# Performance work log

Hardware: AMD Instinct MI355X
Metric: run time of the kernel (lower is better)

The kernel has to match this reference:

```python
import jax, jax.numpy as jnp
import numpy as np

HID = 256
HEADS = 8
HD = HID // HEADS  # head_dim = 32


def setup_inputs() -> dict:
    key = jax.random.key(0)
    ks = jax.random.split(key, 16)
    B, N = 4, 2048
    s = 0.02
    inp = {
        'x': jax.random.normal(ks[0], (B, N, 4, HID), dtype=jnp.float32),
        'Wq': jax.random.normal(ks[1], (HID, HID), dtype=jnp.float32) * s,
        'bq': jnp.zeros((HID,), jnp.float32),
        'Wk': jax.random.normal(ks[2], (HID, HID), dtype=jnp.float32) * s,
        'bk': jnp.zeros((HID,), jnp.float32),
        'Wv': jax.random.normal(ks[3], (HID, HID), dtype=jnp.float32) * s,
        'bv': jnp.zeros((HID,), jnp.float32),
        'Wvec': jax.random.normal(ks[4], (2 * HID, HID), dtype=jnp.float32) * s,
        'Wo': jax.random.normal(ks[5], (3 * HID, HID), dtype=jnp.float32) * s,
        'bo': jnp.zeros((3 * HID,), jnp.float32),
        'Wg': jax.random.normal(ks[6], (HID, 2 * HID), dtype=jnp.float32) * s,
        'bg': jnp.zeros((HID,), jnp.float32),
        'alpha_dot': jnp.asarray(1.0, jnp.float32),
        'alpha_norm': jnp.asarray(1.0, jnp.float32),
    }
    return inp


def reference(x, Wq, bq, Wk, bk, Wv, bv, Wvec, Wo, bo, Wg, bg, alpha_dot, alpha_norm):
    B, N, _, H = x.shape
    nh, hd = HEADS, HD
    x_scalar = x[:, :, 0]          # (B,N,H)
    vec = x[:, :, 1:]              # (B,N,3,H)

    def lin(a, W, b=None):
        y = a @ W.T
        return y + b if b is not None else y

    # scalar q/k/v -> (B,heads,N,hd)
    q = lin(x_scalar, Wq, bq).reshape(B, N, nh, hd).transpose(0, 2, 1, 3)
    k = lin(x_scalar, Wk, bk).reshape(B, N, nh, hd).transpose(0, 2, 1, 3)
    v = lin(x_scalar, Wv, bv).reshape(B, N, nh, hd).transpose(0, 2, 1, 3)

    # invariant features from vector channels
    vec_proj = lin(vec, Wvec)                  # (B,N,3,2H)
    vec1, vec2 = vec_proj[..., :H], vec_proj[..., H:]
    vec_dot = jnp.sum(vec1 * vec2, axis=-2)    # (B,N,H)
    vec_norm = jnp.linalg.norm(vec, axis=2)    # (B,N,H)

    # equivariant values: (B,heads,N,3*hd)
    vec_v = vec.reshape(B, N, 3, nh, hd).transpose(0, 3, 1, 2, 4).reshape(B, nh, N, 3 * hd)

    # fused attention: one softmax, aggregate scalar v and vector v together
    scale = 1.0 / np.sqrt(hd).astype(np.float32)
    scores = jnp.einsum('bhqd,bhkd->bhqk', q, k) * scale
    attn = jax.nn.softmax(scores, axis=-1)
    v_all = jnp.concatenate([v, vec_v], axis=-1)        # (B,h,N,4*hd)
    out_all = jnp.einsum('bhqk,bhkd->bhqd', attn, v_all)
    out_s, out_v = out_all[..., :hd], out_all[..., hd:]

    x_out = out_s.transpose(0, 2, 1, 3).reshape(B, N, H)
    vec_aggr = out_v.reshape(B, nh, N, 3, hd).transpose(0, 2, 3, 1, 4).reshape(B, N, 3, H)

    invariants = jnp.concatenate([alpha_dot * vec_dot, alpha_norm * vec_norm], axis=-1)
    gate = jax.nn.sigmoid(lin(invariants, Wg, bg))[:, :, None, :]  # (B,N,1,H)
    vec_combined = gate * vec_aggr + vec  # vector_mixing='add', gating=True

    o = lin(x_out, Wo, bo)
    o1, o2, o3 = o[..., :H], o[..., H:2 * H], o[..., 2 * H:]
    x_updated = vec_dot * o1 + vec_norm * o2 + o3

    x_final = jnp.concatenate([x_updated[:, :, None, :], vec_combined], axis=2)  # (B,N,4,H)
    return x_final
```

## Files before the change

kernel.cpp:

```cpp
#include <hip/hip_runtime.h>
#include <cstdint>
#include <cstddef>

#define HIDN 256
#define NHEAD 8
#define HD 32
#define NSEQ 2048
#define QS (0.17677669529663687f * 1.4426950408889634f)

typedef __attribute__((ext_vector_type(8))) short short8;
typedef __attribute__((ext_vector_type(4))) short short4v;
typedef __attribute__((ext_vector_type(4))) float f32x4;

static __device__ __forceinline__ short f2bf(float f) {
    union { float f; uint32_t u; } v; v.f = f;
    uint32_t r = (v.u + 0x7FFF + ((v.u >> 16) & 1)) >> 16;
    return (short)r;
}
static __device__ __forceinline__ float bf2f(short s) {
    union { uint32_t u; float f; } v; v.u = ((uint32_t)(uint16_t)s) << 16;
    return v.f;
}

static __device__ __forceinline__ float ex2(float x) {
#if defined(__has_builtin)
#if __has_builtin(__builtin_amdgcn_exp2f)
    return __builtin_amdgcn_exp2f(x);
#else
    return exp2f(x);
#endif
#else
    return exp2f(x);
#endif
}

static __device__ __forceinline__ uint32_t pkbf16(float lo, float hi) {
    uint32_t r;
    asm("v_cvt_pk_bf16_f32 %0, %1, %2" : "=v"(r) : "v"(lo), "v"(hi));
    return r;
}

static __device__ __forceinline__ void gload16(const void* g, void* l) {
    __builtin_amdgcn_global_load_lds(
        (__attribute__((address_space(1))) void*)g,
        (__attribute__((address_space(3))) void*)l, 16, 0, 0);
}

__global__ __launch_bounds__(256) void wcvt_kernel(
    const float* __restrict__ Wq, const float* __restrict__ Wk,
    const float* __restrict__ Wv, const float* __restrict__ Wvec,
    const float* __restrict__ Wo, const float* __restrict__ Wg,
    const float* __restrict__ bq, const float* __restrict__ bk,
    const float* __restrict__ bv,
    const float* __restrict__ ad, const float* __restrict__ an,
    short* __restrict__ Wqkvb, short* __restrict__ Wvecb,
    short* __restrict__ Wob, short* __restrict__ Wgb, float* __restrict__ bqkvs)
{
    int idx = blockIdx.x * 256 + threadIdx.x;
    if (idx < 65536)        Wqkvb[idx] = f2bf(Wq[idx] * QS);
    else if (idx < 131072)  Wqkvb[idx] = f2bf(Wk[idx - 65536]);
    else if (idx < 196608)  Wqkvb[idx] = f2bf(Wv[idx - 131072]);
    else if (idx < 327680)  Wvecb[idx - 196608] = f2bf(Wvec[idx - 196608]);
    else if (idx < 524288)  Wob[idx - 327680] = f2bf(Wo[idx - 327680]);
    else {
        int i2 = idx - 524288;
        int k = i2 & 511;
        float s = (k < 256) ? ad[0] : an[0];
        Wgb[i2] = f2bf(Wg[i2] * s);
    }
    if (idx < 256)          bqkvs[idx] = bq[idx] * QS;
    else if (idx < 512)     bqkvs[idx] = bk[idx - 256];
    else if (idx < 768)     bqkvs[idx] = bv[idx - 512];
}

__global__ __launch_bounds__(256) void qkv_kernel(
    const float* __restrict__ x, const short* __restrict__ Wqkvb,
    const float* __restrict__ bqkvs,
    short* __restrict__ qbf, short* __restrict__ kbf, short* __restrict__ vtb)
{
    __shared__ short xs[32 * 264];
    __shared__ short vtmp[256 * 34];
    const int tid = threadIdx.x;
    const int m0 = blockIdx.x * 32;
    const int b  = m0 >> 11;
    const int n0 = m0 & 2047;

    #pragma unroll
    for (int l = 0; l < 8; l++) {
        int i = l * 256 + tid;
        int t = i >> 6, j4 = i & 63;
        float4 v = *(const float4*)(x + (size_t)(m0 + t) * 1024 + j4 * 4);
        short4v s = { f2bf(v.x), f2bf(v.y), f2bf(v.z), f2bf(v.w) };
        *(short4v*)&xs[t * 264 + j4 * 4] = s;
    }
    __syncthreads();

    const int wave = tid >> 6, lane = tid & 63;
    const int col = lane & 15, quad = lane >> 4;

    short8 xf[2][8];
    #pragma unroll
    for (int mt = 0; mt < 2; mt++)
        #pragma unroll
        for (int kk = 0; kk < 8; kk++)
            xf[mt][kk] = *(const short8*)&xs[(mt * 16 + col) * 264 + kk * 32 + quad * 8];

    #pragma unroll
    for (int y = 0; y < 3; y++) {
        f32x4 acc[2][4];
        #pragma unroll
        for (int mt = 0; mt < 2; mt++)
            #pragma unroll
            for (int nt = 0; nt < 4; nt++) acc[mt][nt] = (f32x4){0.f,0.f,0.f,0.f};

        const short* Wb = Wqkvb + (size_t)(y * 256 + wave * 64) * 256;
        #pragma unroll
        for (int kk = 0; kk < 8; kk++) {
            #pragma unroll
            for (int nt = 0; nt < 4; nt++) {
                short8 wf = *(const short8*)(Wb + (size_t)(nt * 16 + col) * 256 + kk * 32 + quad * 8);
                #pragma unroll
                for (int mt = 0; mt < 2; mt++)
                    acc[mt][nt] = __builtin_amdgcn_mfma_f32_16x16x32_bf16(wf, xf[mt][kk], acc[mt][nt], 0, 0, 0);
            }
        }

        if (y < 2) {
            short* dst = (y == 0) ? qbf : kbf;
            #pragma unroll
            for (int nt = 0; nt < 4; nt++) {
                int ch = wave * 64 + nt * 16 + quad * 4;
                float4 bi = *(const float4*)&bqkvs[y * 256 + ch];
                int h = ch >> 5, d = ch & 31;
                #pragma unroll
                for (int mt = 0; mt < 2; mt++) {
                    int n = n0 + mt * 16 + col;
                    short4v s = { f2bf(acc[mt][nt][0] + bi.x), f2bf(acc[mt][nt][1] + bi.y),
                                  f2bf(acc[mt][nt][2] + bi.z), f2bf(acc[mt][nt][3] + bi.w) };
                    int dd = (y == 1) ? (((d >> 3) ^ ((n >> 1) & 3)) * 8 + (d & 7)) : d;
                    *(short4v*)(dst + ((size_t)(b * 8 + h) * 2048 + n) * 32 + dd) = s;
                }
            }
        } else {
            #pragma unroll
            for (int nt = 0; nt < 4; nt++) {
                int ch = wave * 64 + nt * 16 + quad * 4;
                float4 bi = *(const float4*)&bqkvs[512 + ch];
                #pragma unroll
                for (int mt = 0; mt < 2; mt++) {
                    int tok = mt * 16 + col;
                    vtmp[(ch + 0) * 34 + tok] = f2bf(acc[mt][nt][0] + bi.x);
                    vtmp[(ch + 1) * 34 + tok] = f2bf(acc[mt][nt][1] + bi.y);
                    vtmp[(ch + 2) * 34 + tok] = f2bf(acc[mt][nt][2] + bi.z);
                    vtmp[(ch + 3) * 34 + tok] = f2bf(acc[mt][nt][3] + bi.w);
                }
            }
        }
    }
    __syncthreads();
    {
        int ch = tid;
        short s[32];
        #pragma unroll
        for (int t = 0; t < 32; t++) s[t] = vtmp[ch * 34 + t];
        int h = ch >> 5, d = ch & 31;
        size_t tile = (size_t)(b * 8 + h) * 32 + (n0 >> 6);
        short* dst = vtb + (tile * 128 + d) * 64;
        int gb = (n0 >> 3) & 4;
        #pragma unroll
        for (int g = 0; g < 4; g++)
            *(short8*)(dst + (((gb + g) ^ (d & 7)) * 8)) = *(short8*)&s[g * 8];
    }
}

__global__ __launch_bounds__(512) void vec_kernel(
    const float* __restrict__ x, const short* __restrict__ Wvecb,
    float* __restrict__ dotb, short* __restrict__ invb,
    float* __restrict__ normb, short* __restrict__ vtb)
{
    __shared__ short vb[3 * 16 * 264];
    const int tid = threadIdx.x;
    const int m0 = blockIdx.x * 16;
    const int b = m0 >> 11, n0 = m0 & 2047;

    #pragma unroll
    for (int p = 0; p < 6; p++) {
        int f4 = p * 512 + tid;
        int t = f4 / 192;
        int rem = f4 - t * 192;
        int c = rem >> 6, j4 = rem & 63;
        float4 v = *(const float4*)(x + (size_t)(m0 + t) * 1024 + 256 + c * 256 + j4 * 4);
        short4v s = { f2bf(v.x), f2bf(v.y), f2bf(v.z), f2bf(v.w) };
        *(short4v*)&vb[(c * 16 + t) * 264 + j4 * 4] = s;
    }
    __syncthreads();

    const int wave = tid >> 6, lane = tid & 63;
    const int col = lane & 15, quad = lane >> 4;
    const int j0 = wave * 32;

    f32x4 d1[3][2], d2[3][2];
    #pragma unroll
    for (int c = 0; c < 3; c++)
        #pragma unroll
        for (int nt = 0; nt < 2; nt++) {
            d1[c][nt] = (f32x4){0.f,0.f,0.f,0.f};
            d2[c][nt] = (f32x4){0.f,0.f,0.f,0.f};
        }

    #pragma unroll
    for (int kk = 0; kk < 8; kk++) {
        short8 w1[2], w2[2];
        #pragma unroll
        for (int nt = 0; nt < 2; nt++) {
            w1[nt] = *(const short8*)&Wvecb[(size_t)(j0 + nt * 16 + col) * 256 + kk * 32 + quad * 8];
            w2[nt] = *(const short8*)&Wvecb[(size_t)(256 + j0 + nt * 16 + col) * 256 + kk * 32 + quad * 8];
        }
        #pragma unroll
        for (int c = 0; c < 3; c++) {
            short8 xf = *(const short8*)&vb[(c * 16 + col) * 264 + kk * 32 + quad * 8];
            #pragma unroll
            for (int nt = 0; nt < 2; nt++) {
                d1[c][nt] = __builtin_amdgcn_mfma_f32_16x16x32_bf16(w1[nt], xf, d1[c][nt], 0, 0, 0);
                d2[c][nt] = __builtin_amdgcn_mfma_f32_16x16x32_bf16(w2[nt], xf, d2[c][nt], 0, 0, 0);
            }
        }
    }
    #pragma unroll
    for (int nt = 0; nt < 2; nt++) {
        f32x4 dac = d1[0][nt] * d2[0][nt] + d1[1][nt] * d2[1][nt] + d1[2][nt] * d2[2][nt];
        float4 o = { dac[0], dac[1], dac[2], dac[3] };
        *(float4*)&dotb[(size_t)(m0 + col) * 256 + j0 + nt * 16 + quad * 4] = o;
        short4v s = { f2bf(dac[0]), f2bf(dac[1]), f2bf(dac[2]), f2bf(dac[3]) };
        *(short4v*)&invb[(size_t)(m0 + col) * 512 + j0 + nt * 16 + quad * 4] = s;
    }

    const int j = tid & 255, tp = tid >> 8;
    const int h = j >> 5, d = j & 31;
    #pragma unroll
    for (int t8 = 0; t8 < 8; t8++) {
        int t = tp * 8 + t8;
        float v0 = bf2f(vb[(0 * 16 + t) * 264 + j]);
        float v1 = bf2f(vb[(1 * 16 + t) * 264 + j]);
        float v2 = bf2f(vb[(2 * 16 + t) * 264 + j]);
        float nm = sqrtf(v0 * v0 + v1 * v1 + v2 * v2);
        normb[(size_t)(m0 + t) * 256 + j] = nm;
        invb[(size_t)(m0 + t) * 512 + 256 + j] = f2bf(nm);
    }
    {
        size_t tile = (size_t)(b * 8 + h) * 32 + (n0 >> 6);
        int gg = ((n0 & 63) >> 3) + tp;
        #pragma unroll
        for (int c = 0; c < 3; c++) {
            short8 s;
            #pragma unroll
            for (int t8 = 0; t8 < 8; t8++) s[t8] = vb[(c * 16 + tp * 8 + t8) * 264 + j];
            int row = 32 + c * 32 + d;
            *(short8*)(vtb + (tile * 128 + row) * 64 + ((gg ^ (d & 7)) * 8)) = s;
        }
    }
}

__global__ __launch_bounds__(256) void attn_kernel(
    const short* __restrict__ qb, const short* __restrict__ kb,
    const short* __restrict__ vtb,
    short* __restrict__ xob, short* __restrict__ ovb)
{
    __shared__ short Ks[2][64 * 32];
    __shared__ short Vs[2][128 * 64];
    __shared__ short Pl[4][2][16 * 40];
    const int tid = threadIdx.x;
    const int wave = tid >> 6, lane = tid & 63;
    const int col = lane & 15, quad = lane >> 4;

    const int D = blockIdx.x;
    const int slot = D >> 3;
    const int bh = (D & 7) + ((slot & 3) << 3);
    const int qt = slot >> 2;
    const int m0 = qt * 128 + wave * 32;
    const int b = bh >> 3, h = bh & 7;

    const short* qbase = qb + (size_t)bh * NSEQ * HD;
    const short* ksrc  = kb + (size_t)bh * NSEQ * HD;
    const short* vsrc  = vtb + (size_t)bh * 32 * 8192;

    short8 qfrag[2];
    #pragma unroll
    for (int s = 0; s < 2; s++)
        qfrag[s] = *(const short8*)(qbase + (size_t)(m0 + s * 16 + col) * 32 + quad * 8);

    f32x4 o[2][8];
    #pragma unroll
    for (int s = 0; s < 2; s++)
        #pragma unroll
        for (int dt = 0; dt < 8; dt++) o[s][dt] = (f32x4){0.f,0.f,0.f,0.f};
    float lrun[2] = {0.f, 0.f};

    const int wb = (tid & 192) * 8;

    auto STAGE = [&](int buf, int t) {
        const short* kp = ksrc + (size_t)t * 2048 + tid * 8;
        gload16(kp, &Ks[buf][wb]);
        const short* vp = vsrc + (size_t)t * 8192 + tid * 8;
        #pragma unroll
        for (int p = 0; p < 4; p++)
            gload16(vp + p * 2048, &Vs[buf][p * 2048 + wb]);
    };

    const int ksw  = (quad ^ ((col >> 1) & 3)) * 8;
    const int vsw0 = (quad ^ (col & 7)) * 8;
    const int vsw1 = ((quad + 4) ^ (col & 7)) * 8;

    STAGE(0, 0);
    __syncthreads();

    for (int kt = 0; kt < 32; kt++) {
        const int cur = kt & 1;
        if (kt < 31) STAGE(cur ^ 1, kt + 1);

        short8 kf[4];
        #pragma unroll
        for (int nt = 0; nt < 4; nt++)
            kf[nt] = *(const short8*)&Ks[cur][(nt * 16 + col) * 32 + ksw];

        #pragma unroll
        for (int s = 0; s < 2; s++) {
            f32x4 sc[4];
            #pragma unroll
            for (int nt = 0; nt < 4; nt++)
                sc[nt] = __builtin_amdgcn_mfma_f32_16x16x32_bf16(
                    kf[nt], qfrag[s], (f32x4){0.f,0.f,0.f,0.f}, 0, 0, 0);
            float rs = 0.f;
            short* pd = &Pl[wave][s][col * 40];
            #pragma unroll
            for (int nt = 0; nt < 4; nt++) {
                float p0 = ex2(sc[nt][0]), p1 = ex2(sc[nt][1]);
                float p2 = ex2(sc[nt][2]), p3 = ex2(sc[nt][3]);
                rs += (p0 + p1) + (p2 + p3);
                uint2 w = { pkbf16(p0, p1), pkbf16(p2, p3) };
                *(uint2*)(pd + nt * 16 + quad * 4) = w;
            }
            lrun[s] += rs;
        }

        #pragma unroll
        for (int c = 0; c < 2; c++) {
            short8 pa[2];
            #pragma unroll
            for (int s = 0; s < 2; s++)
                pa[s] = *(const short8*)&Pl[wave][s][col * 40 + c * 32 + quad * 8];
            const int vsw = c ? vsw1 : vsw0;
            #pragma unroll
            for (int dt = 0; dt < 8; dt++) {
                short8 vf = *(const short8*)&Vs[cur][(dt * 16 + col) * 64 + vsw];
                #pragma unroll
                for (int s = 0; s < 2; s++)
                    o[s][dt] = __builtin_amdgcn_mfma_f32_16x16x32_bf16(vf, pa[s], o[s][dt], 0, 0, 0);
            }
        }
        __syncthreads();
    }

    #pragma unroll
    for (int s = 0; s < 2; s++) {
        float l = lrun[s];
        l += __shfl_xor(l, 16);
        l += __shfl_xor(l, 32);
        float linv = 1.0f / l;

        size_t mg = (size_t)b * 2048 + m0 + s * 16 + col;
        short* xr = xob + mg * 256 + h * 32;
        #pragma unroll
        for (int dt = 0; dt < 2; dt++) {
            short4v sv = { f2bf(o[s][dt][0] * linv), f2bf(o[s][dt][1] * linv),
                           f2bf(o[s][dt][2] * linv), f2bf(o[s][dt][3] * linv) };
            *(short4v*)(xr + dt * 16 + quad * 4) = sv;
        }
        short* vr = ovb + mg * 768 + h * 32;
        #pragma unroll
        for (int dt = 2; dt < 8; dt++) {
            int c = (dt - 2) >> 1, d2 = ((dt - 2) & 1) * 16 + quad * 4;
            short4v sv = { f2bf(o[s][dt][0] * linv), f2bf(o[s][dt][1] * linv),
                           f2bf(o[s][dt][2] * linv), f2bf(o[s][dt][3] * linv) };
            *(short4v*)(vr + c * 256 + d2) = sv;
        }
    }
}

__global__ __launch_bounds__(256, 2) void ogemm_kernel(
    const float* __restrict__ x, const short* __restrict__ xob,
    const short* __restrict__ invb,
    const float* __restrict__ dotb, const float* __restrict__ normb,
    const short* __restrict__ ovb,
    const short* __restrict__ Wob, const short* __restrict__ Wgb,
    const float* __restrict__ bo, const float* __restrict__ bg,
    float* __restrict__ out)
{
    __shared__ __align__(16) union {
        struct { short inv[16 * 520]; short xo[16 * 264]; } in;
        struct { short gate[16 * 264]; short o[16 * 776]; } ob;
    } u;
    const int tid = threadIdx.x;
    const int M0 = blockIdx.x * 16;

    #pragma unroll
    for (int l = 0; l < 4; l++) {
        int i = l * 256 + tid;
        int m = i >> 6, seg = i & 63;
        *(short8*)&u.in.inv[m * 520 + seg * 8] =
            *(const short8*)(invb + (size_t)(M0 + m) * 512 + seg * 8);
    }
    #pragma unroll
    for (int l = 0; l < 2; l++) {
        int i = l * 256 + tid;
        int m = i >> 5, seg = i & 31;
        *(short8*)&u.in.xo[m * 264 + seg * 8] =
            *(const short8*)(xob + (size_t)(M0 + m) * 256 + seg * 8);
    }
    __syncthreads();

    const int wave = tid >> 6, lane = tid & 63;
    const int col = lane & 15, quad = lane >> 4;

    f32x4 acc[16];
    #pragma unroll
    for (int nt = 0; nt < 16; nt++) acc[nt] = (f32x4){0.f,0.f,0.f,0.f};

    if (wave == 0) {
        short8 wbuf[2][16];
        #pragma unroll
        for (int nt = 0; nt < 16; nt++)
            wbuf[0][nt] = *(const short8*)(Wgb + (size_t)(nt * 16 + col) * 512 + quad * 8);
        #pragma unroll
        for (int kk = 0; kk < 16; kk++) {
            if (kk < 15) {
                #pragma unroll
                for (int nt = 0; nt < 16; nt++)
                    wbuf[(kk + 1) & 1][nt] =
                        *(const short8*)(Wgb + (size_t)(nt * 16 + col) * 512 + (kk + 1) * 32 + quad * 8);
            }
            short8 xf = *(const short8*)&u.in.inv[col * 520 + kk * 32 + quad * 8];
            #pragma unroll
            for (int nt = 0; nt < 16; nt++)
                acc[nt] = __builtin_amdgcn_mfma_f32_16x16x32_bf16(wbuf[kk & 1][nt], xf, acc[nt], 0, 0, 0);
        }
    } else {
        const short* Wb = Wob + (size_t)(wave - 1) * 256 * 256;
        short8 wbuf[2][16];
        #pragma unroll
        for (int nt = 0; nt < 16; nt++)
            wbuf[0][nt] = *(const short8*)(Wb + (size_t)(nt * 16 + col) * 256 + quad * 8);
        #pragma unroll
        for (int kk = 0; kk < 8; kk++) {
            if (kk < 7) {
                #pragma unroll
                for (int nt = 0; nt < 16; nt++)
                    wbuf[(kk + 1) & 1][nt] =
                        *(const short8*)(Wb + (size_t)(nt * 16 + col) * 256 + (kk + 1) * 32 + quad * 8);
            }
            short8 xf = *(const short8*)&u.in.xo[col * 264 + kk * 32 + quad * 8];
            #pragma unroll
            for (int nt = 0; nt < 16; nt++)
                acc[nt] = __builtin_amdgcn_mfma_f32_16x16x32_bf16(wbuf[kk & 1][nt], xf, acc[nt], 0, 0, 0);
        }
    }
    __syncthreads();

    if (wave == 0) {
        #pragma unroll
        for (int nt = 0; nt < 16; nt++) {
            int ch = nt * 16 + quad * 4;
            float4 bi = *(const float4*)&bg[ch];
            short4v s = { f2bf(1.f / (1.f + __expf(-(acc[nt][0] + bi.x)))),
                          f2bf(1.f / (1.f + __expf(-(acc[nt][1] + bi.y)))),
                          f2bf(1.f / (1.f + __expf(-(acc[nt][2] + bi.z)))),
                          f2bf(1.f / (1.f + __expf(-(acc[nt][3] + bi.w)))) };
            *(short4v*)&u.ob.gate[col * 264 + ch] = s;
        }
    } else {
        #pragma unroll
        for (int nt = 0; nt < 16; nt++) {
            int ch = (wave - 1) * 256 + nt * 16 + quad * 4;
            float4 bi = *(const float4*)&bo[ch];
            short4v s = { f2bf(acc[nt][0] + bi.x), f2bf(acc[nt][1] + bi.y),
                          f2bf(acc[nt][2] + bi.z), f2bf(acc[nt][3] + bi.w) };
            *(short4v*)&u.ob.o[col * 776 + ch] = s;
        }
    }
    __syncthreads();

    #pragma unroll
    for (int l = 0; l < 16; l++) {
        int idx4 = l * 256 + tid;
        int m = idx4 >> 8;
        int j = (idx4 & 255) * 4;
        size_t mg = (size_t)(M0 + m);
        if (j < 256) {
            float4 dv = *(const float4*)(dotb + mg * 256 + j);
            float4 nv = *(const float4*)(normb + mg * 256 + j);
            short4v o1 = *(short4v*)&u.ob.o[m * 776 + j];
            short4v o2 = *(short4v*)&u.ob.o[m * 776 + 256 + j];
            short4v o3 = *(short4v*)&u.ob.o[m * 776 + 512 + j];
            float4 r;
            r.x = dv.x * bf2f(o1[0]) + nv.x * bf2f(o2[0]) + bf2f(o3[0]);
            r.y = dv.y * bf2f(o1[1]) + nv.y * bf2f(o2[1]) + bf2f(o3[1]);
            r.z = dv.z * bf2f(o1[2]) + nv.z * bf2f(o2[2]) + bf2f(o3[2]);
            r.w = dv.w * bf2f(o1[3]) + nv.w * bf2f(o2[3]) + bf2f(o3[3]);
            *(float4*)(out + mg * 1024 + j) = r;
        } else {
            int c = (j >> 8) - 1, jj = j & 255;
            short4v g4 = *(short4v*)&u.ob.gate[m * 264 + jj];
            short4v av4 = *(const short4v*)(ovb + mg * 768 + c * 256 + jj);
            float4 xv = *(const float4*)(x + mg * 1024 + 256 + c * 256 + jj);
            float4 r = { bf2f(g4[0]) * bf2f(av4[0]) + xv.x, bf2f(g4[1]) * bf2f(av4[1]) + xv.y,
                         bf2f(g4[2]) * bf2f(av4[2]) + xv.z, bf2f(g4[3]) * bf2f(av4[3]) + xv.w };
            *(float4*)(out + mg * 1024 + j) = r;
        }
    }
}

extern "C" void kernel_launch(void* const* d_in, const int* in_sizes, int n_in,
                              void* d_out, int out_size, void* d_ws, size_t ws_size,
                              hipStream_t stream)
{
    const float* x    = (const float*)d_in[0];
    const float* Wq   = (const float*)d_in[1];
    const float* bq   = (const float*)d_in[2];
    const float* Wk   = (const float*)d_in[3];
    const float* bk   = (const float*)d_in[4];
    const float* Wv   = (const float*)d_in[5];
    const float* bv   = (const float*)d_in[6];
    const float* Wvec = (const float*)d_in[7];
    const float* Wo   = (const float*)d_in[8];
    const float* bo   = (const float*)d_in[9];
    const float* Wg   = (const float*)d_in[10];
    const float* bg   = (const float*)d_in[11];
    const float* adp  = (const float*)d_in[12];
    const float* anp  = (const float*)d_in[13];
    float* out = (float*)d_out;

    float* ws    = (float*)d_ws;
    short* qbf   = (short*)ws;
    short* kbf   = (short*)(ws + 1048576);
    short* vtb   = (short*)(ws + 2097152);
    float* dotb  = ws + 6291456;
    float* normb = ws + 8388608;
    short* xob   = (short*)(ws + 10485760);
    short* ovb   = (short*)(ws + 11534336);
    short* invb  = (short*)(ws + 17825792);
    short* Wqkvb = (short*)(ws + 19922944);
    float* bqkvs = ws + 20021248;
    short* Wvecb = (short*)(ws + 20022016);
    short* Wob   = (short*)(ws + 20087552);
    short* Wgb   = (short*)(ws + 20185856);

    wcvt_kernel<<<2560, 256, 0, stream>>>(Wq, Wk, Wv, Wvec, Wo, Wg, bq, bk, bv,
                                          adp, anp, Wqkvb, Wvecb, Wob, Wgb, bqkvs);
    qkv_kernel<<<256, 256, 0, stream>>>(x, Wqkvb, bqkvs, qbf, kbf, vtb);
    vec_kernel<<<512, 512, 0, stream>>>(x, Wvecb, dotb, invb, normb, vtb);
    attn_kernel<<<512, 256, 0, stream>>>(qbf, kbf, vtb, xob, ovb);
    ogemm_kernel<<<512, 256, 0, stream>>>(x, xob, invb, dotb, normb, ovb,
                                          Wob, Wgb, bo, bg, out);
}
```

Measured before the change: 269.0 us.

## Switch attention to 32x32x16 MFMA with register-resident P via permlane swap

Attention now uses 32x32x16 bf16 MFMA instead of 16x16x32. K and V are pre-laid-out in fragment order by the producer kernels, so each lane loads its operand directly from LDS with no swizzle. The softmax probabilities are repacked in registers using v_permlane32_swap instead of a round trip through LDS, which removes the Pl buffer and its LDS traffic. The trade-off is higher accumulator register pressure and strict dependence on the new K/V layout matching the MFMA operand mapping.

Result: faster. 259.7 us (-3.4%).

```diff
diff --git a/kernel.cpp b/kernel.cpp
--- a/kernel.cpp
+++ b/kernel.cpp
@@ -11,6 +11,8 @@
 typedef __attribute__((ext_vector_type(8))) short short8;
 typedef __attribute__((ext_vector_type(4))) short short4v;
 typedef __attribute__((ext_vector_type(4))) float f32x4;
+typedef __attribute__((ext_vector_type(16))) float f32x16;
+typedef __attribute__((ext_vector_type(4))) uint32_t u32x4;
 
 static __device__ __forceinline__ short f2bf(float f) {
     union { float f; uint32_t u; } v; v.f = f;
@@ -40,10 +42,23 @@
     return r;
 }
 
+static __device__ __forceinline__ void half_bcast(uint32_t x, uint32_t& lo, uint32_t& hi) {
+    uint32_t a = x, b = x;
+    asm("v_permlane32_swap_b32 %0, %1" : "+v"(a), "+v"(b));
+    lo = a; hi = b;
+}
+
 static __device__ __forceinline__ void gload16(const void* g, void* l) {
     __builtin_amdgcn_global_load_lds(
         (__attribute__((address_space(1))) void*)g,
         (__attribute__((address_space(3))) void*)l, 16, 0, 0);
+}
+
+static __device__ __forceinline__ f32x16 zero16() {
+    f32x16 z;
+    #pragma unroll
+    for (int i = 0; i < 16; i++) z[i] = 0.f;
+    return z;
 }
 
 __global__ __launch_bounds__(256) void wcvt_kernel(
@@ -125,20 +140,36 @@
             }
         }
 
-        if (y < 2) {
-            short* dst = (y == 0) ? qbf : kbf;
+        if (y == 0) {
             #pragma unroll
             for (int nt = 0; nt < 4; nt++) {
                 int ch = wave * 64 + nt * 16 + quad * 4;
-                float4 bi = *(const float4*)&bqkvs[y * 256 + ch];
+                float4 bi = *(const float4*)&bqkvs[ch];
                 int h = ch >> 5, d = ch & 31;
                 #pragma unroll
                 for (int mt = 0; mt < 2; mt++) {
                     int n = n0 + mt * 16 + col;
                     short4v s = { f2bf(acc[mt][nt][0] + bi.x), f2bf(acc[mt][nt][1] + bi.y),
                                   f2bf(acc[mt][nt][2] + bi.z), f2bf(acc[mt][nt][3] + bi.w) };
-                    int dd = (y == 1) ? (((d >> 3) ^ ((n >> 1) & 3)) * 8 + (d & 7)) : d;
-                    *(short4v*)(dst + ((size_t)(b * 8 + h) * 2048 + n) * 32 + dd) = s;
+                    *(short4v*)(qbf + ((size_t)(b * 8 + h) * 2048 + n) * 32 + d) = s;
+                }
+            }
+        } else if (y == 1) {
+            #pragma unroll
+            for (int nt = 0; nt < 4; nt++) {
+                int ch = wave * 64 + nt * 16 + quad * 4;
+                float4 bi = *(const float4*)&bqkvs[256 + ch];
+                int h = ch >> 5, d = ch & 31;
+                #pragma unroll
+                for (int mt = 0; mt < 2; mt++) {
+                    int n = n0 + mt * 16 + col;
+                    short4v s = { f2bf(acc[mt][nt][0] + bi.x), f2bf(acc[mt][nt][1] + bi.y),
+                                  f2bf(acc[mt][nt][2] + bi.z), f2bf(acc[mt][nt][3] + bi.w) };
+                    int f  = ((n & 63) >> 5) * 2 + (d >> 4);
+                    int lk = (n & 31) + (((d >> 3) & 1) << 5);
+                    short* dst = kbf + ((size_t)(b * 8 + h) * 32 + (n >> 6)) * 2048
+                               + f * 512 + lk * 8 + (d & 7);
+                    *(short4v*)dst = s;
                 }
             }
         } else {
@@ -165,11 +196,14 @@
         for (int t = 0; t < 32; t++) s[t] = vtmp[ch * 34 + t];
         int h = ch >> 5, d = ch & 31;
         size_t tile = (size_t)(b * 8 + h) * 32 + (n0 >> 6);
-        short* dst = vtb + (tile * 128 + d) * 64;
-        int gb = (n0 >> 3) & 4;
-        #pragma unroll
-        for (int g = 0; g < 4; g++)
-            *(short8*)(dst + (((gb + g) ^ (d & 7)) * 8)) = *(short8*)&s[g * 8];
+        short* dst = vtb + tile * 8192;
+        #pragma unroll
+        for (int g = 0; g < 4; g++) {
+            int kbse = (n0 & 63) + g * 8;
+            int f = kbse >> 4;
+            int h2 = (kbse >> 3) & 1;
+            *(short8*)(dst + f * 512 + (d + h2 * 32) * 8) = *(short8*)&s[g * 8];
+        }
     }
 }
 
@@ -249,14 +283,15 @@
     }
     {
         size_t tile = (size_t)(b * 8 + h) * 32 + (n0 >> 6);
-        int gg = ((n0 & 63) >> 3) + tp;
+        int kbse = (n0 & 63) + tp * 8;
+        int ks = kbse >> 4, h2 = (kbse >> 3) & 1;
         #pragma unroll
         for (int c = 0; c < 3; c++) {
             short8 s;
             #pragma unroll
             for (int t8 = 0; t8 < 8; t8++) s[t8] = vb[(c * 16 + tp * 8 + t8) * 264 + j];
-            int row = 32 + c * 32 + d;
-            *(short8*)(vtb + (tile * 128 + row) * 64 + ((gg ^ (d & 7)) * 8)) = s;
+            int f = (1 + c) * 4 + ks;
+            *(short8*)(vtb + tile * 8192 + f * 512 + (d + h2 * 32) * 8) = s;
         }
     }
 }
@@ -266,12 +301,11 @@
     const short* __restrict__ vtb,
     short* __restrict__ xob, short* __restrict__ ovb)
 {
-    __shared__ short Ks[2][64 * 32];
-    __shared__ short Vs[2][128 * 64];
-    __shared__ short Pl[4][2][16 * 40];
+    __shared__ short Ks[2][2048];
+    __shared__ short Vs[2][8192];
     const int tid = threadIdx.x;
     const int wave = tid >> 6, lane = tid & 63;
-    const int col = lane & 15, quad = lane >> 4;
+    const int q32 = lane & 31, hi = lane >> 5;
 
     const int D = blockIdx.x;
     const int slot = D >> 3;
@@ -281,35 +315,26 @@
     const int b = bh >> 3, h = bh & 7;
 
     const short* qbase = qb + (size_t)bh * NSEQ * HD;
-    const short* ksrc  = kb + (size_t)bh * NSEQ * HD;
+    const short* ksrc  = kb + (size_t)bh * 32 * 2048;
     const short* vsrc  = vtb + (size_t)bh * 32 * 8192;
 
     short8 qfrag[2];
     #pragma unroll
-    for (int s = 0; s < 2; s++)
-        qfrag[s] = *(const short8*)(qbase + (size_t)(m0 + s * 16 + col) * 32 + quad * 8);
-
-    f32x4 o[2][8];
-    #pragma unroll
-    for (int s = 0; s < 2; s++)
-        #pragma unroll
-        for (int dt = 0; dt < 8; dt++) o[s][dt] = (f32x4){0.f,0.f,0.f,0.f};
-    float lrun[2] = {0.f, 0.f};
-
-    const int wb = (tid & 192) * 8;
+    for (int ks = 0; ks < 2; ks++)
+        qfrag[ks] = *(const short8*)(qbase + (size_t)(m0 + q32) * 32 + ks * 16 + hi * 8);
+
+    f32x16 o[4];
+    #pragma unroll
+    for (int dt = 0; dt < 4; dt++) o[dt] = zero16();
+    float lrun = 0.f;
 
     auto STAGE = [&](int buf, int t) {
-        const short* kp = ksrc + (size_t)t * 2048 + tid * 8;
-        gload16(kp, &Ks[buf][wb]);
+        gload16(ksrc + (size_t)t * 2048 + tid * 8, &Ks[buf][wave * 512]);
         const short* vp = vsrc + (size_t)t * 8192 + tid * 8;
         #pragma unroll
         for (int p = 0; p < 4; p++)
-            gload16(vp + p * 2048, &Vs[buf][p * 2048 + wb]);
+            gload16(vp + p * 2048, &Vs[buf][p * 2048 + wave * 512]);
     };
-
-    const int ksw  = (quad ^ ((col >> 1) & 3)) * 8;
-    const int vsw0 = (quad ^ (col & 7)) * 8;
-    const int vsw1 = ((quad + 4) ^ (col & 7)) * 8;
 
     STAGE(0, 0);
     __syncthreads();
@@ -318,71 +343,70 @@
         const int cur = kt & 1;
         if (kt < 31) STAGE(cur ^ 1, kt + 1);
 
-        short8 kf[4];
-        #pragma unroll
-        for (int nt = 0; nt < 4; nt++)
-            kf[nt] = *(const short8*)&Ks[cur][(nt * 16 + col) * 32 + ksw];
-
-        #pragma unroll
-        for (int s = 0; s < 2; s++) {
-            f32x4 sc[4];
-            #pragma unroll
-            for (int nt = 0; nt < 4; nt++)
-                sc[nt] = __builtin_amdgcn_mfma_f32_16x16x32_bf16(
-                    kf[nt], qfrag[s], (f32x4){0.f,0.f,0.f,0.f}, 0, 0, 0);
-            float rs = 0.f;
-            short* pd = &Pl[wave][s][col * 40];
-            #pragma unroll
-            for (int nt = 0; nt < 4; nt++) {
-                float p0 = ex2(sc[nt][0]), p1 = ex2(sc[nt][1]);
-                float p2 = ex2(sc[nt][2]), p3 = ex2(sc[nt][3]);
-                rs += (p0 + p1) + (p2 + p3);
-                uint2 w = { pkbf16(p0, p1), pkbf16(p2, p3) };
-                *(uint2*)(pd + nt * 16 + quad * 4) = w;
-            }
-            lrun[s] += rs;
-        }
-
-        #pragma unroll
-        for (int c = 0; c < 2; c++) {
-            short8 pa[2];
-            #pragma unroll
-            for (int s = 0; s < 2; s++)
-                pa[s] = *(const short8*)&Pl[wave][s][col * 40 + c * 32 + quad * 8];
-            const int vsw = c ? vsw1 : vsw0;
-            #pragma unroll
-            for (int dt = 0; dt < 8; dt++) {
-                short8 vf = *(const short8*)&Vs[cur][(dt * 16 + col) * 64 + vsw];
-                #pragma unroll
-                for (int s = 0; s < 2; s++)
-                    o[s][dt] = __builtin_amdgcn_mfma_f32_16x16x32_bf16(vf, pa[s], o[s][dt], 0, 0, 0);
+        f32x16 sc[2];
+        #pragma unroll
+        for (int t = 0; t < 2; t++) {
+            f32x16 a = zero16();
+            #pragma unroll
+            for (int ks = 0; ks < 2; ks++) {
+                short8 kf = *(const short8*)&Ks[cur][(t * 2 + ks) * 512 + lane * 8];
+                a = __builtin_amdgcn_mfma_f32_32x32x16_bf16(kf, qfrag[ks], a, 0, 0, 0);
+            }
+            sc[t] = a;
+        }
+
+        uint32_t alo[2][4], ahi[2][4], blo[2][4], bhi[2][4];
+        float rs = 0.f;
+        #pragma unroll
+        for (int t = 0; t < 2; t++) {
+            float e[16];
+            #pragma unroll
+            for (int r = 0; r < 16; r++) { e[r] = ex2(sc[t][r]); rs += e[r]; }
+            #pragma unroll
+            for (int g = 0; g < 4; g++) {
+                half_bcast(pkbf16(e[4*g+0], e[4*g+1]), alo[t][g], ahi[t][g]);
+                half_bcast(pkbf16(e[4*g+2], e[4*g+3]), blo[t][g], bhi[t][g]);
+            }
+        }
+        lrun += rs;
+
+        #pragma unroll
+        for (int s = 0; s < 4; s++) {
+            const int t = s >> 1, g0 = (s & 1) * 2, g1 = g0 + 1;
+            uint32_t u0 = hi ? alo[t][g1] : alo[t][g0];
+            uint32_t u1 = hi ? blo[t][g1] : blo[t][g0];
+            uint32_t u2 = hi ? ahi[t][g1] : ahi[t][g0];
+            uint32_t u3 = hi ? bhi[t][g1] : bhi[t][g0];
+            u32x4 pv = { u0, u1, u2, u3 };
+            short8 pf = __builtin_bit_cast(short8, pv);
+            #pragma unroll
+            for (int dt = 0; dt < 4; dt++) {
+                short8 vf = *(const short8*)&Vs[cur][(dt * 4 + s) * 512 + lane * 8];
+                o[dt] = __builtin_amdgcn_mfma_f32_32x32x16_bf16(vf, pf, o[dt], 0, 0, 0);
             }
         }
         __syncthreads();
     }
 
-    #pragma unroll
-    for (int s = 0; s < 2; s++) {
-        float l = lrun[s];
-        l += __shfl_xor(l, 16);
-        l += __shfl_xor(l, 32);
-        float linv = 1.0f / l;
-
-        size_t mg = (size_t)b * 2048 + m0 + s * 16 + col;
-        short* xr = xob + mg * 256 + h * 32;
-        #pragma unroll
-        for (int dt = 0; dt < 2; dt++) {
-            short4v sv = { f2bf(o[s][dt][0] * linv), f2bf(o[s][dt][1] * linv),
-                           f2bf(o[s][dt][2] * linv), f2bf(o[s][dt][3] * linv) };
-            *(short4v*)(xr + dt * 16 + quad * 4) = sv;
-        }
-        short* vr = ovb + mg * 768 + h * 32;
-        #pragma unroll
-        for (int dt = 2; dt < 8; dt++) {
-            int c = (dt - 2) >> 1, d2 = ((dt - 2) & 1) * 16 + quad * 4;
-            short4v sv = { f2bf(o[s][dt][0] * linv), f2bf(o[s][dt][1] * linv),
-                           f2bf(o[s][dt][2] * linv), f2bf(o[s][dt][3] * linv) };
-            *(short4v*)(vr + c * 256 + d2) = sv;
+    float l = lrun + __shfl_xor(lrun, 32);
+    float linv = 1.0f / l;
+
+    size_t mg = (size_t)b * 2048 + m0 + q32;
+    short* xr = xob + mg * 256 + h * 32;
+    #pragma unroll
+    for (int g = 0; g < 4; g++) {
+        short4v sv = { f2bf(o[0][4*g+0] * linv), f2bf(o[0][4*g+1] * linv),
+                       f2bf(o[0][4*g+2] * linv), f2bf(o[0][4*g+3] * linv) };
+        *(short4v*)(xr + g * 8 + hi * 4) = sv;
+    }
+    short* vr = ovb + mg * 768 + h * 32;
+    #pragma unroll
+    for (int dt = 1; dt < 4; dt++) {
+        #pragma unroll
+        for (int g = 0; g < 4; g++) {
+            short4v sv = { f2bf(o[dt][4*g+0] * linv), f2bf(o[dt][4*g+1] * linv),
+                           f2bf(o[dt][4*g+2] * linv), f2bf(o[dt][4*g+3] * linv) };
+            *(short4v*)(vr + (dt - 1) * 256 + g * 8 + hi * 4) = sv;
         }
     }
 }
```
